# Performance work log

Measured on AMD Instinct MI355X. Metric: run time of the kernel, lower is better.

Reference implementation:

```python
import jax, jax.numpy as jnp
import numpy as np

C = 3          # num_classes
A = 3          # num_anchors per cell
IMG = 1024.0
W_LOC, W_OBJ, W_CLS = 2.0, 1.0, 1.0
POS_T, NEG_T, HNM_RATIO = 0.5, 0.3, 3


def _make_anchors(H, W, stride):
    ys = (np.arange(H) + 0.5) * stride
    xs = (np.arange(W) + 0.5) * stride
    cy, cx = np.meshgrid(ys, xs, indexing='ij')
    sizes = np.array([2.0, 3.0, 4.0]) * stride          # A anchor scales
    cx = cx[:, :, None]; cy = cy[:, :, None]; s = sizes[None, None, :]
    a = np.stack([cx - s / 2, cy - s / 2, cx + s / 2, cy + s / 2], axis=-1)  # [H,W,A,4]
    return jnp.asarray(a.reshape(-1, 4), dtype=jnp.float32)


def setup_inputs() -> dict:
    key = jax.random.key(0)
    k1, k2, k3, k4, k5, k6 = jax.random.split(key, 6)
    B, M = 32, 20
    p1 = jax.random.normal(k1, (B, A * (5 + C), 128, 128), jnp.float32)
    p2 = jax.random.normal(k2, (B, A * (5 + C), 64, 64), jnp.float32)
    p3 = jax.random.normal(k3, (B, A * (5 + C), 32, 32), jnp.float32)
    anchors1 = _make_anchors(128, 128, 8)
    anchors2 = _make_anchors(64, 64, 16)
    anchors3 = _make_anchors(32, 32, 32)
    cxy = jax.random.uniform(k4, (B, M, 2), minval=0.0, maxval=IMG)
    wh = jax.random.uniform(k5, (B, M, 2), minval=16.0, maxval=256.0)
    boxes = jnp.clip(jnp.concatenate([cxy - wh / 2, cxy + wh / 2], -1), 0.0, IMG)
    labels = jax.random.randint(k6, (B, M), 0, C + 1)  # 0 = padding, 1..C = class
    return {"p1": p1, "p2": p2, "p3": p3,
            "anchors1": anchors1, "anchors2": anchors2, "anchors3": anchors3,
            "boxes": boxes, "labels": labels}


def _iou(anchors, boxes):
    # anchors [N,4], boxes [M,4], xyxy -> [N,M]
    lt = jnp.maximum(anchors[:, None, :2], boxes[None, :, :2])
    rb = jnp.minimum(anchors[:, None, 2:], boxes[None, :, 2:])
    wh = jnp.maximum(rb - lt, 0.0)
    inter = wh[..., 0] * wh[..., 1]
    area_a = (anchors[:, 2] - anchors[:, 0]) * (anchors[:, 3] - anchors[:, 1])
    area_b = (boxes[:, 2] - boxes[:, 0]) * (boxes[:, 3] - boxes[:, 1])
    return inter / jnp.maximum(area_a[:, None] + area_b[None, :] - inter, 1e-9)


def _decode(pred):
    # yolo_decode: [B, A*(5+C), H, W] -> deltas [B,N,4], obj [B,N], cls [B,N,C]; N = H*W*A
    B, _, H, W = pred.shape
    p = pred.reshape(B, A, 5 + C, H, W).transpose(0, 3, 4, 1, 2).reshape(B, H * W * A, 5 + C)
    return p[..., :4], p[..., 4], p[..., 5:]


def _level_loss(deltas, obj_logits, cls_logits, anchors, boxes, labels):
    # single image, single level
    valid = (labels > 0)
    iou = _iou(anchors, boxes) * valid[None, :].astype(deltas.dtype)
    best_iou = iou.max(axis=1)
    best_idx = iou.argmax(axis=1)
    pos = best_iou >= POS_T
    neg = best_iou < NEG_T
    mboxes = boxes[best_idx]
    mlabels = labels[best_idx]
    posf = pos.astype(deltas.dtype)
    # SmoothL1 (beta=1), mean over 4 coords, summed over positives
    d = jnp.abs(deltas - mboxes)
    sl1 = jnp.where(d < 1.0, 0.5 * d * d, d - 0.5).mean(axis=-1)
    loc = jnp.sum(sl1 * posf)
    # BCEWithLogits against objectness targets (= pos mask)
    x = obj_logits
    bce = jnp.maximum(x, 0.0) - x * posf + jnp.log1p(jnp.exp(-jnp.abs(x)))
    # hard negative mining on detached obj loss
    num_pos = pos.sum()
    num_neg = neg.sum()
    k = jnp.where(num_pos == 0,
                  jnp.minimum(100, num_neg),
                  jnp.minimum(num_pos * HNM_RATIO, num_neg))
    masked = jnp.where(neg, jax.lax.stop_gradient(bce), -1e9)
    order = jnp.argsort(-masked)
    ranks = jnp.zeros_like(order).at[order].set(jnp.arange(order.shape[0]))
    sel = (ranks < k) & neg
    obj = jnp.sum(bce * (pos | sel).astype(bce.dtype))
    # CrossEntropy over positives, labels shifted by -1
    logp = jax.nn.log_softmax(cls_logits, axis=-1)
    tgt = jnp.clip(mlabels - 1, 0, C - 1)
    nll = -jnp.take_along_axis(logp, tgt[:, None], axis=1)[:, 0]
    cls = jnp.sum(nll * posf)
    return loc, obj, cls, num_pos, sel.sum()


def reference(p1, p2, p3, anchors1, anchors2, anchors3, boxes, labels):
    total_loc = total_obj = total_cls = 0.0
    total_pos = total_neg = 0
    for pred, anchors in ((p1, anchors1), (p2, anchors2), (p3, anchors3)):
        deltas, obj_l, cls_l = _decode(pred)
        loc, obj, cls, npos, nneg = jax.vmap(
            _level_loss, in_axes=(0, 0, 0, None, 0, 0)
        )(deltas, obj_l, cls_l, anchors, boxes, labels)
        total_loc = total_loc + loc.sum()
        total_obj = total_obj + obj.sum()
        total_cls = total_cls + cls.sum()
        total_pos = total_pos + npos.sum()
        total_neg = total_neg + nneg.sum()
    norm = jnp.maximum(total_pos + total_neg, 1).astype(jnp.float32)
    loss_loc = W_LOC * total_loc / norm
    loss_obj = W_OBJ * total_obj / norm
    loss_cls = W_CLS * total_cls / jnp.maximum(total_pos, 1).astype(jnp.float32)
    return loss_loc + loss_obj + loss_cls, loss_loc, loss_obj, loss_cls
```

## Files before the change

### kernel.cpp

```cpp
#include <hip/hip_runtime.h>

#define NB 32
#define NM 20
#define NA 3
#define NCH 8
#define N0 49152
#define N1 12288
#define N2 3072


__device__ __forceinline__ float wredf(float v) {
  #pragma unroll
  for (int o = 32; o; o >>= 1) v += __shfl_down(v, o, 64);
  return v;
}

__device__ __forceinline__ float softplus_neg_abs(float x) {
  return __logf(1.0f + __expf(-fabsf(x)));
}

__device__ __forceinline__ float blockredf(float v, float* swred, int tid) {
  v = wredf(v);
  if ((tid & 63) == 0) swred[tid >> 6] = v;
  __syncthreads();
  float s = 0.f;
  if (tid == 0) {
    #pragma unroll
    for (int i = 0; i < 16; ++i) s += swred[i];
  }
  __syncthreads();
  return s;
}

__device__ __forceinline__ unsigned suffix1024(unsigned* scan, int tid) {
  #pragma unroll
  for (int d = 1; d < 1024; d <<= 1) {
    unsigned t = (tid + d < 1024) ? scan[tid + d] : 0u;
    __syncthreads();
    scan[tid] += t;
    __syncthreads();
  }
  return scan[tid];
}

__global__ __launch_bounds__(256, 8) void kA(
    const float* __restrict__ pr0, const float* __restrict__ pr1,
    const float* __restrict__ pr2,
    const float* __restrict__ boxes, const int* __restrict__ labels,
    unsigned* __restrict__ keys, float* __restrict__ partials)
{
  const int bx = blockIdx.x, b = blockIdx.y, tid = threadIdx.x;
  int blk, wshift, HW, nblk, koff, poff; float stride; const float* pred;
  if (bx < 64)      { blk = bx;      wshift = 7; HW = 16384; nblk = 64; koff = 0;            poff = 0;                         stride = 8.f;  pred = pr0; }
  else if (bx < 80) { blk = bx - 64; wshift = 6; HW = 4096;  nblk = 16; koff = NB * N0;      poff = NB * 64 * 5;               stride = 16.f; pred = pr1; }
  else              { blk = bx - 80; wshift = 5; HW = 1024;  nblk = 4;  koff = NB * (N0+N1); poff = NB * 64 * 5 + NB * 16 * 5; stride = 32.f; pred = pr2; }

  const int   nrows = 256 >> wshift;
  const int   h0    = blk * nrows;
  const float ymin  = ((float)h0 + 0.5f) * stride - 2.f * stride;
  const float ymax  = ((float)(h0 + nrows - 1) + 0.5f) * stride + 2.f * stride;

  __shared__ float sbx1[NM], sby1[NM], sbx2[NM], sby2[NM], sarea[NM];
  __shared__ int   slab[NM];
  __shared__ int   s_nv;
  if (tid < 64) {
    float x1 = 0, y1 = 0, x2 = 0, y2 = 0; int lb = 0; bool v = false;
    if (tid < NM) {
      x1 = boxes[(b * NM + tid) * 4 + 0];
      y1 = boxes[(b * NM + tid) * 4 + 1];
      x2 = boxes[(b * NM + tid) * 4 + 2];
      y2 = boxes[(b * NM + tid) * 4 + 3];
      lb = labels[b * NM + tid];
      v  = (lb > 0) && (y2 > ymin) && (y1 < ymax);
    }
    unsigned long long mask = __ballot(v);
    int pref = __popcll(mask & ((1ull << tid) - 1ull));
    if (v) {
      sbx1[pref] = x1; sby1[pref] = y1; sbx2[pref] = x2; sby2[pref] = y2;
      sarea[pref] = (x2 - x1) * (y2 - y1);
      slab[pref]  = lb;
    }
    if (tid == 0) s_nv = (int)__popcll(mask);
  }
  __syncthreads();

  const int hw = blk * 256 + tid;
  const int W  = 1 << wshift;
  const int w  = hw & (W - 1);
  const int h  = hw >> wshift;
  const float cx = ((float)w + 0.5f) * stride;
  const float cy = ((float)h + 0.5f) * stride;
  const float* pb = pred + (size_t)b * (NA * NCH) * HW + hw;

  float xo[NA];
  #pragma unroll
  for (int a = 0; a < NA; ++a) xo[a] = pb[(a * NCH + 4) * HW];

  float ax1[NA], ay1[NA], ax2[NA], ay2[NA], aar[NA];
  #pragma unroll
  for (int a = 0; a < NA; ++a) {
    const float s  = (2.0f + (float)a) * stride;
    const float hx = 0.5f * s;
    ax1[a] = cx - hx; ax2[a] = cx + hx;
    ay1[a] = cy - hx; ay2[a] = cy + hx;
    aar[a] = s * s;
  }

  float best[NA] = {0.f, 0.f, 0.f};
  int   bidx[NA] = {0, 0, 0};
  const int nv = s_nv;

  for (int m = 0; m < nv; ++m) {
    const float bx1 = sbx1[m], by1 = sby1[m], bx2 = sbx2[m], by2 = sby2[m];
    const float ba  = sarea[m];
    float inter_[NA], un_[NA];
    #pragma unroll
    for (int a = 0; a < NA; ++a) {
      float ix = fminf(ax2[a], bx2) - fmaxf(ax1[a], bx1);
      float iy = fminf(ay2[a], by2) - fmaxf(ay1[a], by1);
      inter_[a] = fmaxf(ix, 0.f) * fmaxf(iy, 0.f);
      un_[a]    = aar[a] + ba - inter_[a];
    }
    if (__any(inter_[NA - 1] > 0.f)) {
      #pragma unroll
      for (int a = 0; a < NA; ++a) {
        float iou = inter_[a] / fmaxf(un_[a], 1e-9f);
        if (iou > best[a]) { best[a] = iou; bidx[a] = m; }
      }
    }
  }

  float loc_s = 0.f, obj_s = 0.f, cls_s = 0.f;
  float pos_c = 0.f, neg_c = 0.f;
  const int kbase = koff + b * (HW * NA) + hw * NA;

  #pragma unroll
  for (int a = 0; a < NA; ++a) {
    const bool pos = best[a] >= 0.5f;
    const bool neg = best[a] < 0.3f;
    const float x  = xo[a];
    const float sp = softplus_neg_abs(x);

    unsigned key = 0u;
    if (pos) {
      const int m = bidx[a];
      pos_c += 1.f;
      obj_s += fmaxf(x, 0.f) - x + sp;
      float tb[4] = {sbx1[m], sby1[m], sbx2[m], sby2[m]};
      float ls = 0.f;
      #pragma unroll
      for (int c = 0; c < 4; ++c) {
        float d = fabsf(pb[(a * NCH + c) * HW] - tb[c]);
        ls += (d < 1.f) ? 0.5f * d * d : (d - 0.5f);
      }
      loc_s += 0.25f * ls;
      float l0 = pb[(a * NCH + 5) * HW];
      float l1 = pb[(a * NCH + 6) * HW];
      float l2 = pb[(a * NCH + 7) * HW];
      float mx  = fmaxf(fmaxf(l0, l1), l2);
      float lse = mx + __logf(__expf(l0 - mx) + __expf(l1 - mx) + __expf(l2 - mx));
      int tgt = slab[m] - 1; tgt = tgt < 0 ? 0 : (tgt > 2 ? 2 : tgt);
      float lt = (tgt == 0) ? l0 : ((tgt == 1) ? l1 : l2);
      cls_s += lse - lt;
    } else if (neg) {
      neg_c += 1.f;
      float bn = fmaxf(x, 0.f) + sp;
      key = __float_as_uint(bn) | 0x80000000u;
    }
    keys[kbase + a] = key;
  }

  loc_s = wredf(loc_s); obj_s = wredf(obj_s); cls_s = wredf(cls_s);
  pos_c = wredf(pos_c); neg_c = wredf(neg_c);
  __shared__ float sred[4][5];
  const int wv = tid >> 6;
  if ((tid & 63) == 0) {
    sred[wv][0] = loc_s; sred[wv][1] = obj_s; sred[wv][2] = cls_s;
    sred[wv][3] = pos_c; sred[wv][4] = neg_c;
  }
  __syncthreads();
  if (tid == 0) {
    float* slot = partials + poff + (size_t)(b * nblk + blk) * 5;
    #pragma unroll
    for (int j = 0; j < 5; ++j)
      slot[j] = sred[0][j] + sred[1][j] + sred[2][j] + sred[3][j];
  }
}

template<int NL4, bool GUARD>
__device__ float kb_core(const unsigned* __restrict__ kp, int n4, unsigned k,
                         unsigned* hist, unsigned* scan, float* fsum,
                         float* swred, unsigned* sh_sel, unsigned* sh_r, int tid)
{
  const uint4* kp4 = (const uint4*)kp;
  uint4 v[NL4];

  for (int i = tid; i < 4096; i += 1024) hist[i] = 0u;
  __syncthreads();

  #pragma unroll
  for (int j = 0; j < NL4; ++j)
    if (!GUARD || tid + j * 1024 < n4) v[j] = kp4[tid + j * 1024];

  #pragma unroll
  for (int j = 0; j < NL4; ++j)
    if (!GUARD || tid + j * 1024 < n4) {
      atomicAdd(&hist[v[j].x >> 20], 1u);
      atomicAdd(&hist[v[j].y >> 20], 1u);
      atomicAdd(&hist[v[j].z >> 20], 1u);
      atomicAdd(&hist[v[j].w >> 20], 1u);
    }
  __syncthreads();

  unsigned c0 = hist[tid*4], c1 = hist[tid*4+1], c2 = hist[tid*4+2], c3 = hist[tid*4+3];
  unsigned st = c0 + c1 + c2 + c3;
  scan[tid] = st;
  __syncthreads();
  unsigned I = suffix1024(scan, tid);
  unsigned H = I - st;
  if (H < k && k <= I) {
    unsigned cum = H;
    if (cum + c3 >= k)      { *sh_sel = tid*4+3; *sh_r = k - cum; }
    else { cum += c3;
      if (cum + c2 >= k)    { *sh_sel = tid*4+2; *sh_r = k - cum; }
      else { cum += c2;
        if (cum + c1 >= k)  { *sh_sel = tid*4+1; *sh_r = k - cum; }
        else { cum += c1;     *sh_sel = tid*4;   *sh_r = k - cum; } } }
  }
  __syncthreads();
  const unsigned pref0 = *sh_sel;
  const unsigned r1    = *sh_r;
  __syncthreads();

  hist[tid] = 0u; fsum[tid] = 0.f;
  __syncthreads();
  float s_above = 0.f;
  #pragma unroll
  for (int j = 0; j < NL4; ++j)
    if (!GUARD || tid + j * 1024 < n4) {
      #pragma unroll
      for (int cchan = 0; cchan < 4; ++cchan) {
        unsigned u = (&v[j].x)[cchan];
        unsigned d = u >> 20;
        float val = __uint_as_float(u & 0x7fffffffu);
        if (d > pref0) s_above += val;
        else if (d == pref0) {
          unsigned s2 = (u >> 10) & 1023u;
          atomicAdd(&hist[s2], 1u);
          atomicAdd(&fsum[s2], val);
        }
      }
    }
  __syncthreads();
  float S0 = blockredf(s_above, swred, tid);

  unsigned cc = hist[tid];
  scan[tid] = cc;
  __syncthreads();
  unsigned I1 = suffix1024(scan, tid);
  unsigned H1 = I1 - cc;
  if (H1 < r1 && r1 <= I1) { *sh_sel = tid; *sh_r = r1 - H1; }
  __syncthreads();
  const unsigned sel1 = *sh_sel;
  const unsigned r2   = *sh_r;
  float S1 = blockredf(tid > (int)sel1 ? fsum[tid] : 0.f, swred, tid);

  hist[tid] = 0u; fsum[tid] = 0.f;
  __syncthreads();
  const unsigned pref01 = (pref0 << 10) | sel1;
  #pragma unroll
  for (int j = 0; j < NL4; ++j)
    if (!GUARD || tid + j * 1024 < n4) {
      #pragma unroll
      for (int cchan = 0; cchan < 4; ++cchan) {
        unsigned u = (&v[j].x)[cchan];
        if ((u >> 10) == pref01) {
          unsigned s2 = u & 1023u;
          atomicAdd(&hist[s2], 1u);
          atomicAdd(&fsum[s2], __uint_as_float(u & 0x7fffffffu));
        }
      }
    }
  __syncthreads();

  cc = hist[tid];
  scan[tid] = cc;
  __syncthreads();
  unsigned I2 = suffix1024(scan, tid);
  unsigned H2 = I2 - cc;
  if (H2 < r2 && r2 <= I2) { *sh_sel = tid; *sh_r = r2 - H2; }
  __syncthreads();
  const unsigned sel2 = *sh_sel;
  const unsigned r3   = *sh_r;
  float S2 = blockredf(tid > (int)sel2 ? fsum[tid] : 0.f, swred, tid);

  const unsigned T = (pref01 << 10) | sel2;
  const float Tval = __uint_as_float(T & 0x7fffffffu);
  return S0 + S1 + S2 + Tval * (float)r3;
}

__global__ __launch_bounds__(1024) void kB(const unsigned* __restrict__ keys,
                                           const float* __restrict__ partials,
                                           float* __restrict__ finals)
{
  __shared__ unsigned hist[4096];
  __shared__ unsigned scan[1024];
  __shared__ float    fsum[1024];
  __shared__ float    swred[16];
  __shared__ float    gp[5];
  __shared__ unsigned sh_sel, sh_r;

  const int bl = blockIdx.x, lvl = bl / NB, b = bl % NB, tid = threadIdx.x;
  const int NLs[3]   = {N0, N1, N2};
  const int BASEs[3] = {0, NB * N0, NB * (N0 + N1)};
  const int NSL[3]   = {64, 16, 4};
  const int POFF[3]  = {0, NB * 64 * 5, NB * 64 * 5 + NB * 16 * 5};

  if (tid < 64) {
    float v0=0,v1=0,v2=0,v3=0,v4=0;
    if (tid < NSL[lvl]) {
      const float* pp = partials + POFF[lvl] + (size_t)(b * NSL[lvl] + tid) * 5;
      v0=pp[0]; v1=pp[1]; v2=pp[2]; v3=pp[3]; v4=pp[4];
    }
    v0=wredf(v0); v1=wredf(v1); v2=wredf(v2); v3=wredf(v3); v4=wredf(v4);
    if (tid==0){gp[0]=v0;gp[1]=v1;gp[2]=v2;gp[3]=v3;gp[4]=v4;}
  }
  __syncthreads();
  const int np = (int)gp[3], nn = (int)gp[4];
  const int k  = (np == 0) ? (nn < 100 ? nn : 100)
                           : (np * 3 < nn ? np * 3 : nn);

  float topk = 0.f;
  if (k > 0) {
    const unsigned* kp = keys + BASEs[lvl] + (size_t)b * NLs[lvl];
    if (lvl == 0)      topk = kb_core<12,false>(kp, 12288, (unsigned)k, hist, scan, fsum, swred, &sh_sel, &sh_r, tid);
    else if (lvl == 1) topk = kb_core<3, false>(kp, 3072,  (unsigned)k, hist, scan, fsum, swred, &sh_sel, &sh_r, tid);
    else               topk = kb_core<1, true >(kp, 768,   (unsigned)k, hist, scan, fsum, swred, &sh_sel, &sh_r, tid);
  }
  if (tid == 0) {
    float* f = finals + (size_t)bl * 5;
    f[0] = gp[0];
    f[1] = gp[1] + topk;
    f[2] = gp[2];
    f[3] = gp[3];
    f[4] = (float)k;
  }
}

__global__ void kC(const float* __restrict__ finals, float* __restrict__ out)
{
  const int tid = threadIdx.x;
  float loc = 0.f, obj = 0.f, cls = 0.f, pos = 0.f, sel = 0.f;
  if (tid < 96) {
    const float* f = finals + (size_t)tid * 5;
    loc = f[0]; obj = f[1]; cls = f[2]; pos = f[3]; sel = f[4];
  }
  loc = wredf(loc); obj = wredf(obj); cls = wredf(cls);
  pos = wredf(pos); sel = wredf(sel);
  __shared__ float sf[5][2];
  const int wv = tid >> 6;
  if ((tid & 63) == 0) { sf[0][wv] = loc; sf[1][wv] = obj; sf[2][wv] = cls;
                         sf[3][wv] = pos; sf[4][wv] = sel; }
  __syncthreads();
  if (tid == 0) {
    float L  = sf[0][0] + sf[0][1];
    float O  = sf[1][0] + sf[1][1];
    float Cl = sf[2][0] + sf[2][1];
    float P  = sf[3][0] + sf[3][1];
    float S  = sf[4][0] + sf[4][1];
    float norm  = fmaxf(P + S, 1.f);
    float l_loc = 2.0f * L / norm;
    float l_obj = O / norm;
    float l_cls = Cl / fmaxf(P, 1.f);
    out[0] = l_loc + l_obj + l_cls;
    out[1] = l_loc;
    out[2] = l_obj;
    out[3] = l_cls;
  }
}

extern "C" void kernel_launch(void* const* d_in, const int* in_sizes, int n_in,
                              void* d_out, int out_size, void* d_ws, size_t ws_size,
                              hipStream_t stream) {
  const float* p1     = (const float*)d_in[0];
  const float* p2     = (const float*)d_in[1];
  const float* p3     = (const float*)d_in[2];
  const float* boxes  = (const float*)d_in[6];
  const int*   labels = (const int*)d_in[7];
  float* out = (float*)d_out;

  char* ws = (char*)d_ws;
  float*    partials = (float*)ws;
  float*    finals   = (float*)(ws + 53760);
  unsigned* keys     = (unsigned*)(ws + 57344);

  kA<<<dim3(84, NB), 256, 0, stream>>>(p1, p2, p3, boxes, labels, keys, partials);
  kB<<<96, 1024, 0, stream>>>(keys, partials, finals);
  kC<<<1, 128, 0, stream>>>(finals, out);
}
```

Baseline: 38.06 us.

## Store box data as float4, drop IoU divides, and coalesce anchor key writes

Box coordinates are packed into float4 shared-memory entries, and the next box is prefetched one iteration ahead. The IoU argmax now cross-multiplies intersection and union instead of dividing, and the positive/negative thresholds are applied the same way. The wave-wide `__any` skip branch is removed. Keys are now written anchor-major (a*HW + hw) so each store is contiguous across threads, which assumes the downstream selection kernel does not depend on key order. Tie-breaking and rounding at the thresholds can differ slightly from the division form.

```diff
diff --git a/kernel.cpp b/kernel.cpp
--- a/kernel.cpp
+++ b/kernel.cpp
@@ -60,9 +60,10 @@
   const float ymin  = ((float)h0 + 0.5f) * stride - 2.f * stride;
   const float ymax  = ((float)(h0 + nrows - 1) + 0.5f) * stride + 2.f * stride;
 
-  __shared__ float sbx1[NM], sby1[NM], sbx2[NM], sby2[NM], sarea[NM];
-  __shared__ int   slab[NM];
-  __shared__ int   s_nv;
+  __shared__ float4 sb4[NM + 1];
+  __shared__ float2 sa2[NM + 1];
+  __shared__ int    slab[NM + 1];
+  __shared__ int    s_nv;
   if (tid < 64) {
     float x1 = 0, y1 = 0, x2 = 0, y2 = 0; int lb = 0; bool v = false;
     if (tid < NM) {
@@ -76,11 +77,16 @@
     unsigned long long mask = __ballot(v);
     int pref = __popcll(mask & ((1ull << tid) - 1ull));
     if (v) {
-      sbx1[pref] = x1; sby1[pref] = y1; sbx2[pref] = x2; sby2[pref] = y2;
-      sarea[pref] = (x2 - x1) * (y2 - y1);
-      slab[pref]  = lb;
-    }
-    if (tid == 0) s_nv = (int)__popcll(mask);
+      sb4[pref] = make_float4(x1, y1, x2, y2);
+      sa2[pref] = make_float2((x2 - x1) * (y2 - y1), 0.f);
+      slab[pref] = lb;
+    }
+    if (tid == 0) {
+      int nv = (int)__popcll(mask);
+      s_nv = nv;
+      sb4[nv] = make_float4(0.f, 0.f, 0.f, 0.f);
+      sa2[nv] = make_float2(0.f, 0.f);
+    }
   }
   __syncthreads();
 
@@ -106,53 +112,53 @@
     aar[a] = s * s;
   }
 
-  float best[NA] = {0.f, 0.f, 0.f};
-  int   bidx[NA] = {0, 0, 0};
+  float bi[NA] = {0.f, 0.f, 0.f};
+  float bu[NA] = {1.f, 1.f, 1.f};
+  int   bm[NA] = {0, 0, 0};
   const int nv = s_nv;
 
+  float4 bb = sb4[0];
+  float2 aa = sa2[0];
   for (int m = 0; m < nv; ++m) {
-    const float bx1 = sbx1[m], by1 = sby1[m], bx2 = sbx2[m], by2 = sby2[m];
-    const float ba  = sarea[m];
-    float inter_[NA], un_[NA];
+    const float4 nb = sb4[m + 1];
+    const float2 na = sa2[m + 1];
     #pragma unroll
     for (int a = 0; a < NA; ++a) {
-      float ix = fminf(ax2[a], bx2) - fmaxf(ax1[a], bx1);
-      float iy = fminf(ay2[a], by2) - fmaxf(ay1[a], by1);
-      inter_[a] = fmaxf(ix, 0.f) * fmaxf(iy, 0.f);
-      un_[a]    = aar[a] + ba - inter_[a];
-    }
-    if (__any(inter_[NA - 1] > 0.f)) {
-      #pragma unroll
-      for (int a = 0; a < NA; ++a) {
-        float iou = inter_[a] / fmaxf(un_[a], 1e-9f);
-        if (iou > best[a]) { best[a] = iou; bidx[a] = m; }
-      }
-    }
+      float ix = fminf(ax2[a], bb.z) - fmaxf(ax1[a], bb.x);
+      float iy = fminf(ay2[a], bb.w) - fmaxf(ay1[a], bb.y);
+      float inter = fmaxf(ix, 0.f) * fmaxf(iy, 0.f);
+      float un = (aar[a] + aa.x) - inter;
+      bool better = inter * bu[a] > bi[a] * un;
+      if (better) { bi[a] = inter; bu[a] = un; bm[a] = m; }
+    }
+    bb = nb; aa = na;
   }
 
   float loc_s = 0.f, obj_s = 0.f, cls_s = 0.f;
   float pos_c = 0.f, neg_c = 0.f;
-  const int kbase = koff + b * (HW * NA) + hw * NA;
 
   #pragma unroll
   for (int a = 0; a < NA; ++a) {
-    const bool pos = best[a] >= 0.5f;
-    const bool neg = best[a] < 0.3f;
+    const bool pos = 2.f * bi[a] >= bu[a];
+    const bool neg = bi[a] < 0.3f * bu[a];
     const float x  = xo[a];
     const float sp = softplus_neg_abs(x);
 
     unsigned key = 0u;
     if (pos) {
-      const int m = bidx[a];
+      const int m = bm[a];
       pos_c += 1.f;
       obj_s += fmaxf(x, 0.f) - x + sp;
-      float tb[4] = {sbx1[m], sby1[m], sbx2[m], sby2[m]};
+      const float4 tb = sb4[m];
       float ls = 0.f;
-      #pragma unroll
-      for (int c = 0; c < 4; ++c) {
-        float d = fabsf(pb[(a * NCH + c) * HW] - tb[c]);
-        ls += (d < 1.f) ? 0.5f * d * d : (d - 0.5f);
-      }
+      float d0 = fabsf(pb[(a * NCH + 0) * HW] - tb.x);
+      float d1 = fabsf(pb[(a * NCH + 1) * HW] - tb.y);
+      float d2 = fabsf(pb[(a * NCH + 2) * HW] - tb.z);
+      float d3 = fabsf(pb[(a * NCH + 3) * HW] - tb.w);
+      ls += (d0 < 1.f) ? 0.5f * d0 * d0 : (d0 - 0.5f);
+      ls += (d1 < 1.f) ? 0.5f * d1 * d1 : (d1 - 0.5f);
+      ls += (d2 < 1.f) ? 0.5f * d2 * d2 : (d2 - 0.5f);
+      ls += (d3 < 1.f) ? 0.5f * d3 * d3 : (d3 - 0.5f);
       loc_s += 0.25f * ls;
       float l0 = pb[(a * NCH + 5) * HW];
       float l1 = pb[(a * NCH + 6) * HW];
@@ -167,7 +173,7 @@
       float bn = fmaxf(x, 0.f) + sp;
       key = __float_as_uint(bn) | 0x80000000u;
     }
-    keys[kbase + a] = key;
+    keys[koff + b * (HW * NA) + a * HW + hw] = key;
   }
 
   loc_s = wredf(loc_s); obj_s = wredf(obj_s); cls_s = wredf(cls_s);
```

Result: no change. 37.89 us (-0.4%).
